# Kernel tuning notes

Hardware: AMD Instinct MI355X
Metric: run time of the kernel (lower is better)

The kernel has to match this reference:

```python
import jax, jax.numpy as jnp
import numpy as np
import math

MIN_NORM = 1e-15
EPS = 4e-3  # float32 boundary eps used by PoincareBall.proj
C = 1.0


def artanh(x):
    x = jnp.clip(x, -1.0 + 1e-7, 1.0 - 1e-7)
    return 0.5 * (jnp.log1p(x) - jnp.log1p(-x))


def _norm(x):
    return jnp.maximum(jnp.linalg.norm(x, axis=-1, keepdims=True), MIN_NORM)


def proj(x, c):
    n = _norm(x)
    maxnorm = (1.0 - EPS) / jnp.sqrt(c)
    return jnp.where(n > maxnorm, x / n * maxnorm, x)


def expmap0(u, c):
    sc = jnp.sqrt(c)
    n = _norm(u)
    return jnp.tanh(sc * n) * u / (sc * n)


def logmap0(p, c):
    sc = jnp.sqrt(c)
    n = _norm(p)
    return artanh(sc * n) * p / (sc * n)


def mobius_add(x, y, c):
    x2 = jnp.sum(x * x, -1, keepdims=True)
    y2 = jnp.sum(y * y, -1, keepdims=True)
    xy = jnp.sum(x * y, -1, keepdims=True)
    num = (1 + 2 * c * xy + c * y2) * x + (1 - c * x2) * y
    den = 1 + 2 * c * xy + c * c * x2 * y2
    return num / jnp.maximum(den, MIN_NORM)


def mobius_matvec(m, x, c):
    sc = jnp.sqrt(c)
    xn = _norm(x)
    mx = x @ m.T
    mxn = _norm(mx)
    res = jnp.tanh(mxn / xn * artanh(sc * xn)) * mx / (mxn * sc)
    zero = jnp.all(mx == 0, axis=-1, keepdims=True)
    return jnp.where(zero, jnp.zeros((), x.dtype), res)


def hnn_layer(x, W, b, c):
    # HypLinear (dropout=0, use_bias=1) followed by HypAct(relu); proj_tan0 is identity for PoincareBall.
    res = proj(mobius_matvec(W, x, c), c)
    hb = proj(expmap0(b.reshape(1, -1), c), c)
    res = proj(mobius_add(res, hb, c), c)
    xt = jax.nn.relu(logmap0(res, c))
    return proj(expmap0(xt, c), c)


def setup_inputs():
    key = jax.random.key(0)
    ks = jax.random.split(key, 5)
    B, N, K, D = 4, 2000, 5, 32
    H1, H2 = 160, 32  # H_layer1: 32 -> 32*5, H_layer2: 32 -> 32
    # points on the Poincare ball (small norm so logmap0 is well-conditioned)
    in_feats = 0.05 * jax.random.normal(ks[0], (B, N, D), jnp.float32)
    # one-hot neighbor adjacency [batch, agent, nei, agent]
    nei_idx = jax.random.randint(ks[1], (B, N, K), 0, N)
    in_nei = jax.nn.one_hot(nei_idx, N, dtype=jnp.float32)
    # xavier_uniform with gain sqrt(2), zero bias (reset_parameters)
    b1w = math.sqrt(2.0) * math.sqrt(6.0 / (H1 + D))
    b2w = math.sqrt(2.0) * math.sqrt(6.0 / (H2 + H2))
    W1 = jax.random.uniform(ks[2], (H1, D), jnp.float32, -b1w, b1w)
    W2 = jax.random.uniform(ks[3], (H2, H2), jnp.float32, -b2w, b2w)
    b1 = jnp.zeros((H1,), jnp.float32)
    b2 = jnp.zeros((H2,), jnp.float32)
    return {"in_feats": in_feats, "in_nei": in_nei, "W1": W1, "b1": b1,
            "W2": W2, "b2": b2, "h_dim": 32, "head": 5}


def reference(in_feats, in_nei, W1, b1, W2, b2, h_dim, head):
    c = C
    B, N, D = in_feats.shape
    K = in_nei.shape[2]
    # tangent-space features (proj_tan0 is identity)
    feats = logmap0(in_feats, c)                                   # [B,N,D]
    agent = proj(expmap0(feats[:, :, None, :], c), c)              # [B,N,1,D]
    # one-hot adjacency gather: equals matmul(in_nei, repeat(feats)) in the torch code
    nbr_t = jnp.einsum('bnkm,bmd->bnkd', in_nei, feats)            # [B,N,K,D]
    nbr = proj(expmap0(nbr_t, c), c)
    # query heads
    q = logmap0(hnn_layer(agent, W1, b1, c), c)                    # [B,N,1,h*head]
    q = q.reshape(B, N, 1, h_dim, head).transpose(0, 1, 4, 2, 3)   # [B,N,head,1,h]
    # key heads; the torch code recomputes H_layer1(neighbor_repr) for values with
    # identical weights/inputs (dropout=0), so values == keys and we reuse them.
    kv = logmap0(hnn_layer(nbr, W1, b1, c), c)
    kv = kv.reshape(B, N, K, h_dim, head).transpose(0, 1, 4, 2, 3)  # [B,N,head,K,h]
    att = jax.nn.softmax(jnp.einsum('bnhqd,bnhkd->bnhqk', q, kv), axis=-1)  # [B,N,head,1,K]
    att_record = att.reshape(B, N, head, K)
    out = jnp.einsum('bnhqk,bnhkd->bnhqd', att, kv).mean(axis=2)   # [B,N,1,h]
    out = out.reshape(B, N, h_dim)
    out = proj(expmap0(out, c), c)
    out = hnn_layer(out, W2, b2, c)                                # [B,N,32]
    return out, att_record
```

## Files before the change

### kernel.cpp

```cpp
#include <hip/hip_runtime.h>
#include <math.h>

#define BB 4
#define NN 2000
#define KK 5
#define DD 32
#define H1 160
#define HEAD 5
#define HDIM 32
#define MAXNORM 0.996f
#define MINN 1e-15f

__device__ __forceinline__ float artanh_f(float x) {
    x = fminf(fmaxf(x, -1.0f + 1e-7f), 1.0f - 1e-7f);
    return 0.5f * (log1pf(x) - log1pf(-x));
}

__device__ __forceinline__ float wave_sum(float v) {
#pragma unroll
    for (int o = 32; o > 0; o >>= 1) v += __shfl_xor(v, o, 64);
    return v;
}

__global__ __launch_bounds__(256) void find_idx_kernel(const float* __restrict__ nei,
                                                       int* __restrict__ idx) {
    const int total4 = BB * NN * KK * NN / 4;
    int stride = gridDim.x * blockDim.x;
    for (int i = blockIdx.x * blockDim.x + threadIdx.x; i < total4; i += stride) {
        float4 v = ((const float4*)nei)[i];
        int f = -1;
        if (v.x > 0.5f) f = 0;
        if (v.y > 0.5f) f = 1;
        if (v.z > 0.5f) f = 2;
        if (v.w > 0.5f) f = 3;
        if (f >= 0) {
            int flat = i * 4 + f;
            int row = flat / NN;
            int m = flat - row * NN;
            idx[row] = m;
        }
    }
}

__global__ __launch_bounds__(256) void g_kernel(const float* __restrict__ xin,
                                                const float* __restrict__ W1,
                                                const float* __restrict__ b1,
                                                float* __restrict__ g) {
    int wave = (blockIdx.x * blockDim.x + threadIdx.x) >> 6;
    int lane = threadIdx.x & 63;
    if (wave >= BB * NN) return;
    bool j2ok = lane < (H1 - 128);

    float x = (lane < DD) ? xin[wave * DD + lane] : 0.f;

    float n = fmaxf(sqrtf(wave_sum(x * x)), MINN);
    float f = (artanh_f(n) / n) * x;
    float fn = fmaxf(sqrtf(wave_sum(f * f)), MINN);
    float p = (tanhf(fn) / fn) * f;
    float pn = fmaxf(sqrtf(wave_sum(p * p)), MINN);
    if (pn > MAXNORM) p *= MAXNORM / pn;
    float xn = fmaxf(sqrtf(wave_sum(p * p)), MINN);

    float mx0 = 0.f, mx1 = 0.f, mx2 = 0.f;
#pragma unroll
    for (int d = 0; d < DD; ++d) {
        float pd = __shfl(p, d, 64);
        mx0 += W1[lane * DD + d] * pd;
        mx1 += W1[(lane + 64) * DD + d] * pd;
        if (j2ok) mx2 += W1[(lane + 128) * DD + d] * pd;
    }
    float m2 = mx0 * mx0 + mx1 * mx1 + (j2ok ? mx2 * mx2 : 0.f);
    float mxn = fmaxf(sqrtf(wave_sum(m2)), MINN);
    float sc = tanhf(mxn / xn * artanh_f(xn)) / mxn;
    float r0 = sc * mx0, r1 = sc * mx1, r2 = sc * mx2;
    float rn = fmaxf(sqrtf(wave_sum(r0 * r0 + r1 * r1 + (j2ok ? r2 * r2 : 0.f))), MINN);
    if (rn > MAXNORM) { float s = MAXNORM / rn; r0 *= s; r1 *= s; r2 *= s; }

    float bb0 = b1[lane], bb1 = b1[lane + 64], bb2 = j2ok ? b1[lane + 128] : 0.f;
    float bn = fmaxf(sqrtf(wave_sum(bb0 * bb0 + bb1 * bb1 + bb2 * bb2)), MINN);
    float bs = tanhf(bn) / bn;
    float h0 = bs * bb0, h1 = bs * bb1, h2 = bs * bb2;
    float hn = fmaxf(sqrtf(wave_sum(h0 * h0 + h1 * h1 + h2 * h2)), MINN);
    if (hn > MAXNORM) { float s = MAXNORM / hn; h0 *= s; h1 *= s; h2 *= s; }

    float x2s = wave_sum(r0 * r0 + r1 * r1 + (j2ok ? r2 * r2 : 0.f));
    float y2s = wave_sum(h0 * h0 + h1 * h1 + h2 * h2);
    float xys = wave_sum(r0 * h0 + r1 * h1 + (j2ok ? r2 * h2 : 0.f));
    float ca = 1.f + 2.f * xys + y2s;
    float cb = 1.f - x2s;
    float den = fmaxf(1.f + 2.f * xys + x2s * y2s, MINN);
    float a0 = (ca * r0 + cb * h0) / den;
    float a1 = (ca * r1 + cb * h1) / den;
    float a2 = (ca * r2 + cb * h2) / den;
    float an = fmaxf(sqrtf(wave_sum(a0 * a0 + a1 * a1 + (j2ok ? a2 * a2 : 0.f))), MINN);
    if (an > MAXNORM) { float s = MAXNORM / an; a0 *= s; a1 *= s; a2 *= s; }

    float ln = fmaxf(sqrtf(wave_sum(a0 * a0 + a1 * a1 + (j2ok ? a2 * a2 : 0.f))), MINN);
    float ls = artanh_f(ln) / ln;
    float t0 = fmaxf(ls * a0, 0.f), t1 = fmaxf(ls * a1, 0.f), t2 = fmaxf(ls * a2, 0.f);
    float tn = fmaxf(sqrtf(wave_sum(t0 * t0 + t1 * t1 + (j2ok ? t2 * t2 : 0.f))), MINN);
    float es = tanhf(tn) / tn;
    float y0 = es * t0, y1 = es * t1, y2 = es * t2;
    float yn = fmaxf(sqrtf(wave_sum(y0 * y0 + y1 * y1 + (j2ok ? y2 * y2 : 0.f))), MINN);
    if (yn > MAXNORM) { float s = MAXNORM / yn; y0 *= s; y1 *= s; y2 *= s; }
    float gn = fmaxf(sqrtf(wave_sum(y0 * y0 + y1 * y1 + (j2ok ? y2 * y2 : 0.f))), MINN);
    float gs = artanh_f(gn) / gn;

    float* go = g + (size_t)wave * H1;
    go[lane] = gs * y0;
    go[lane + 64] = gs * y1;
    if (j2ok) go[lane + 128] = gs * y2;
}

__global__ __launch_bounds__(256) void att_kernel(const float* __restrict__ g,
                                                  const int* __restrict__ idx,
                                                  float* __restrict__ att_out) {
    int t = blockIdx.x * blockDim.x + threadIdx.x;
    if (t >= BB * NN * HEAD) return;
    int h = t % HEAD;
    int r = t / HEAD;
    int b = r / NN;

    const float* gq = g + (size_t)r * H1;
    float q[HDIM];
#pragma unroll
    for (int d = 0; d < HDIM; ++d) q[d] = gq[d * HEAD + h];

    float s[KK];
#pragma unroll
    for (int k = 0; k < KK; ++k) {
        int m = idx[r * KK + k];
        const float* gk = g + (size_t)(b * NN + m) * H1;
        float acc = 0.f;
#pragma unroll
        for (int d = 0; d < HDIM; ++d) acc += q[d] * gk[d * HEAD + h];
        s[k] = acc;
    }
    float mxv = s[0];
#pragma unroll
    for (int k = 1; k < KK; ++k) mxv = fmaxf(mxv, s[k]);
    float e[KK], sum = 0.f;
#pragma unroll
    for (int k = 0; k < KK; ++k) { e[k] = expf(s[k] - mxv); sum += e[k]; }
    float inv = 1.f / sum;
#pragma unroll
    for (int k = 0; k < KK; ++k) att_out[t * KK + k] = e[k] * inv;
}

__global__ __launch_bounds__(256) void out_kernel(const float* __restrict__ g,
                                                  const int* __restrict__ idx,
                                                  const float* __restrict__ att,
                                                  const float* __restrict__ W2,
                                                  const float* __restrict__ b2,
                                                  float* __restrict__ out) {
    int r = blockIdx.x * blockDim.x + threadIdx.x;
    if (r >= BB * NN) return;
    int b = r / NN;

    float o[HDIM];
#pragma unroll
    for (int d = 0; d < HDIM; ++d) o[d] = 0.f;
#pragma unroll
    for (int k = 0; k < KK; ++k) {
        int m = idx[r * KK + k];
        const float* gk = g + (size_t)(b * NN + m) * H1;
#pragma unroll
        for (int h = 0; h < HEAD; ++h) {
            float a = att[(r * HEAD + h) * KK + k];
#pragma unroll
            for (int d = 0; d < HDIM; ++d) o[d] += a * gk[d * HEAD + h];
        }
    }
#pragma unroll
    for (int d = 0; d < HDIM; ++d) o[d] *= (1.f / HEAD);

    float n2 = 0.f;
#pragma unroll
    for (int d = 0; d < HDIM; ++d) n2 += o[d] * o[d];
    float n = fmaxf(sqrtf(n2), MINN);
    float es = tanhf(n) / n;
#pragma unroll
    for (int d = 0; d < HDIM; ++d) o[d] *= es;
    n2 = 0.f;
#pragma unroll
    for (int d = 0; d < HDIM; ++d) n2 += o[d] * o[d];
    n = fmaxf(sqrtf(n2), MINN);
    if (n > MAXNORM) {
        float s = MAXNORM / n;
#pragma unroll
        for (int d = 0; d < HDIM; ++d) o[d] *= s;
    }

    float xn2 = 0.f;
#pragma unroll
    for (int d = 0; d < HDIM; ++d) xn2 += o[d] * o[d];
    float xn = fmaxf(sqrtf(xn2), MINN);
    float mx[HDIM];
#pragma unroll
    for (int j = 0; j < HDIM; ++j) {
        float acc = 0.f;
#pragma unroll
        for (int d = 0; d < HDIM; ++d) acc += W2[j * HDIM + d] * o[d];
        mx[j] = acc;
    }
    float mxn2 = 0.f;
#pragma unroll
    for (int j = 0; j < HDIM; ++j) mxn2 += mx[j] * mx[j];
    float mxn = fmaxf(sqrtf(mxn2), MINN);
    float sc = tanhf(mxn / xn * artanh_f(xn)) / mxn;
#pragma unroll
    for (int j = 0; j < HDIM; ++j) mx[j] *= sc;
    float rn2 = 0.f;
#pragma unroll
    for (int j = 0; j < HDIM; ++j) rn2 += mx[j] * mx[j];
    float rn = fmaxf(sqrtf(rn2), MINN);
    if (rn > MAXNORM) {
        float s = MAXNORM / rn;
#pragma unroll
        for (int j = 0; j < HDIM; ++j) mx[j] *= s;
    }

    float hb[HDIM];
    float bn2 = 0.f;
#pragma unroll
    for (int j = 0; j < HDIM; ++j) { hb[j] = b2[j]; bn2 += hb[j] * hb[j]; }
    float bn = fmaxf(sqrtf(bn2), MINN);
    float bs = tanhf(bn) / bn;
    float hn2 = 0.f;
#pragma unroll
    for (int j = 0; j < HDIM; ++j) { hb[j] *= bs; hn2 += hb[j] * hb[j]; }
    float hn = fmaxf(sqrtf(hn2), MINN);
    if (hn > MAXNORM) {
        float s = MAXNORM / hn;
#pragma unroll
        for (int j = 0; j < HDIM; ++j) hb[j] *= s;
    }
    float x2s = 0.f, y2s = 0.f, xys = 0.f;
#pragma unroll
    for (int j = 0; j < HDIM; ++j) {
        x2s += mx[j] * mx[j];
        y2s += hb[j] * hb[j];
        xys += mx[j] * hb[j];
    }
    float ca = 1.f + 2.f * xys + y2s;
    float cb = 1.f - x2s;
    float den = fmaxf(1.f + 2.f * xys + x2s * y2s, MINN);
    float a[HDIM];
#pragma unroll
    for (int j = 0; j < HDIM; ++j) a[j] = (ca * mx[j] + cb * hb[j]) / den;
    float an2 = 0.f;
#pragma unroll
    for (int j = 0; j < HDIM; ++j) an2 += a[j] * a[j];
    float an = fmaxf(sqrtf(an2), MINN);
    if (an > MAXNORM) {
        float s = MAXNORM / an;
#pragma unroll
        for (int j = 0; j < HDIM; ++j) a[j] *= s;
    }
    float ln2 = 0.f;
#pragma unroll
    for (int j = 0; j < HDIM; ++j) ln2 += a[j] * a[j];
    float lnn = fmaxf(sqrtf(ln2), MINN);
    float ls = artanh_f(lnn) / lnn;
#pragma unroll
    for (int j = 0; j < HDIM; ++j) a[j] = fmaxf(ls * a[j], 0.f);
    float tn2 = 0.f;
#pragma unroll
    for (int j = 0; j < HDIM; ++j) tn2 += a[j] * a[j];
    float tn = fmaxf(sqrtf(tn2), MINN);
    float es2 = tanhf(tn) / tn;
#pragma unroll
    for (int j = 0; j < HDIM; ++j) a[j] *= es2;
    float yn2 = 0.f;
#pragma unroll
    for (int j = 0; j < HDIM; ++j) yn2 += a[j] * a[j];
    float yn = fmaxf(sqrtf(yn2), MINN);
    if (yn > MAXNORM) {
        float s = MAXNORM / yn;
#pragma unroll
        for (int j = 0; j < HDIM; ++j) a[j] *= s;
    }
#pragma unroll
    for (int j = 0; j < HDIM; ++j) out[(size_t)r * HDIM + j] = a[j];
}

extern "C" void kernel_launch(void* const* d_in, const int* in_sizes, int n_in,
                              void* d_out, int out_size, void* d_ws, size_t ws_size,
                              hipStream_t stream) {
    const float* in_feats = (const float*)d_in[0];
    const float* in_nei = (const float*)d_in[1];
    const float* W1 = (const float*)d_in[2];
    const float* b1 = (const float*)d_in[3];
    const float* W2 = (const float*)d_in[4];
    const float* b2 = (const float*)d_in[5];

    int* idx = (int*)d_ws;
    size_t idx_bytes = ((size_t)BB * NN * KK * sizeof(int) + 255) & ~(size_t)255;
    float* g = (float*)((char*)d_ws + idx_bytes);

    float* out = (float*)d_out;
    float* att = out + (size_t)BB * NN * HDIM;

    hipLaunchKernelGGL(find_idx_kernel, dim3(4096), dim3(256), 0, stream, in_nei, idx);
    hipLaunchKernelGGL(g_kernel, dim3((BB * NN * 64 + 255) / 256), dim3(256), 0, stream,
                       in_feats, W1, b1, g);
    hipLaunchKernelGGL(att_kernel, dim3((BB * NN * HEAD + 255) / 256), dim3(256), 0, stream,
                       g, idx, att);
    hipLaunchKernelGGL(out_kernel, dim3((BB * NN + 255) / 256), dim3(256), 0, stream,
                       g, idx, att, W2, b2, out);
}
```

Baseline: 594.8 us.

## Fuse attention and output kernels wave-per-row; early-exit one-hot index search

Merges the attention-softmax kernel and the output kernel into one kernel that uses a 64-lane wave per agent row. The 32 feature dimensions are spread across lanes and reduced with cross-lane shuffles, replacing per-thread 32-element register arrays and strided gathers. The intermediate attention buffer is no longer written and re-read. The index finder now assigns one wave per one-hot row and stops at the first chunk holding the 1, which avoids scanning the rest of the adjacency row. That early exit assumes each row contains exactly one nonzero.

```diff
diff --git a/kernel.cpp b/kernel.cpp
--- a/kernel.cpp
+++ b/kernel.cpp
@@ -22,22 +22,34 @@
     return v;
 }
 
+__device__ __forceinline__ float wave_sum32(float v) {
+#pragma unroll
+    for (int o = 16; o > 0; o >>= 1) v += __shfl_xor(v, o, 64);
+    return v;
+}
+
 __global__ __launch_bounds__(256) void find_idx_kernel(const float* __restrict__ nei,
                                                        int* __restrict__ idx) {
-    const int total4 = BB * NN * KK * NN / 4;
-    int stride = gridDim.x * blockDim.x;
-    for (int i = blockIdx.x * blockDim.x + threadIdx.x; i < total4; i += stride) {
-        float4 v = ((const float4*)nei)[i];
-        int f = -1;
-        if (v.x > 0.5f) f = 0;
-        if (v.y > 0.5f) f = 1;
-        if (v.z > 0.5f) f = 2;
-        if (v.w > 0.5f) f = 3;
-        if (f >= 0) {
-            int flat = i * 4 + f;
-            int row = flat / NN;
-            int m = flat - row * NN;
-            idx[row] = m;
+    int wave = (blockIdx.x * blockDim.x + threadIdx.x) >> 6;
+    int lane = threadIdx.x & 63;
+    if (wave >= BB * NN * KK) return;
+    const float* row = nei + (size_t)wave * NN;
+#pragma unroll 1
+    for (int it = 0; it < 8; ++it) {
+        int base = it * 256 + lane * 4;
+        bool found = false;
+        int pos = 0;
+        if (base < NN) {
+            float4 v = *(const float4*)(row + base);
+            if (v.x > 0.5f) { found = true; pos = base; }
+            if (v.y > 0.5f) { found = true; pos = base + 1; }
+            if (v.z > 0.5f) { found = true; pos = base + 2; }
+            if (v.w > 0.5f) { found = true; pos = base + 3; }
+        }
+        unsigned long long m = __ballot(found);
+        if (m) {
+            if (found) idx[wave] = pos;
+            break;
         }
     }
 }
@@ -112,176 +124,103 @@
     if (j2ok) go[lane + 128] = gs * y2;
 }
 
-__global__ __launch_bounds__(256) void att_kernel(const float* __restrict__ g,
-                                                  const int* __restrict__ idx,
-                                                  float* __restrict__ att_out) {
-    int t = blockIdx.x * blockDim.x + threadIdx.x;
-    if (t >= BB * NN * HEAD) return;
-    int h = t % HEAD;
-    int r = t / HEAD;
+__global__ __launch_bounds__(256) void fused_att_out_kernel(const float* __restrict__ g,
+                                                            const int* __restrict__ idx,
+                                                            const float* __restrict__ W2,
+                                                            const float* __restrict__ b2,
+                                                            float* __restrict__ out,
+                                                            float* __restrict__ att_out) {
+    int wave = (blockIdx.x * blockDim.x + threadIdx.x) >> 6;
+    int lane = threadIdx.x & 63;
+    if (wave >= BB * NN) return;
+    int r = wave;
     int b = r / NN;
+    int d = lane & 31;
 
     const float* gq = g + (size_t)r * H1;
-    float q[HDIM];
-#pragma unroll
-    for (int d = 0; d < HDIM; ++d) q[d] = gq[d * HEAD + h];
-
-    float s[KK];
+    float q[HEAD];
+#pragma unroll
+    for (int h = 0; h < HEAD; ++h) q[h] = gq[d * HEAD + h];
+
+    float kv[KK][HEAD];
+    float s[KK][HEAD];
 #pragma unroll
     for (int k = 0; k < KK; ++k) {
         int m = idx[r * KK + k];
         const float* gk = g + (size_t)(b * NN + m) * H1;
-        float acc = 0.f;
-#pragma unroll
-        for (int d = 0; d < HDIM; ++d) acc += q[d] * gk[d * HEAD + h];
-        s[k] = acc;
-    }
-    float mxv = s[0];
-#pragma unroll
-    for (int k = 1; k < KK; ++k) mxv = fmaxf(mxv, s[k]);
-    float e[KK], sum = 0.f;
-#pragma unroll
-    for (int k = 0; k < KK; ++k) { e[k] = expf(s[k] - mxv); sum += e[k]; }
-    float inv = 1.f / sum;
-#pragma unroll
-    for (int k = 0; k < KK; ++k) att_out[t * KK + k] = e[k] * inv;
-}
-
-__global__ __launch_bounds__(256) void out_kernel(const float* __restrict__ g,
-                                                  const int* __restrict__ idx,
-                                                  const float* __restrict__ att,
-                                                  const float* __restrict__ W2,
-                                                  const float* __restrict__ b2,
-                                                  float* __restrict__ out) {
-    int r = blockIdx.x * blockDim.x + threadIdx.x;
-    if (r >= BB * NN) return;
-    int b = r / NN;
-
-    float o[HDIM];
-#pragma unroll
-    for (int d = 0; d < HDIM; ++d) o[d] = 0.f;
-#pragma unroll
-    for (int k = 0; k < KK; ++k) {
-        int m = idx[r * KK + k];
-        const float* gk = g + (size_t)(b * NN + m) * H1;
-#pragma unroll
-        for (int h = 0; h < HEAD; ++h) {
-            float a = att[(r * HEAD + h) * KK + k];
-#pragma unroll
-            for (int d = 0; d < HDIM; ++d) o[d] += a * gk[d * HEAD + h];
-        }
-    }
-#pragma unroll
-    for (int d = 0; d < HDIM; ++d) o[d] *= (1.f / HEAD);
-
-    float n2 = 0.f;
-#pragma unroll
-    for (int d = 0; d < HDIM; ++d) n2 += o[d] * o[d];
-    float n = fmaxf(sqrtf(n2), MINN);
-    float es = tanhf(n) / n;
-#pragma unroll
-    for (int d = 0; d < HDIM; ++d) o[d] *= es;
-    n2 = 0.f;
-#pragma unroll
-    for (int d = 0; d < HDIM; ++d) n2 += o[d] * o[d];
-    n = fmaxf(sqrtf(n2), MINN);
-    if (n > MAXNORM) {
-        float s = MAXNORM / n;
-#pragma unroll
-        for (int d = 0; d < HDIM; ++d) o[d] *= s;
-    }
-
-    float xn2 = 0.f;
-#pragma unroll
-    for (int d = 0; d < HDIM; ++d) xn2 += o[d] * o[d];
-    float xn = fmaxf(sqrtf(xn2), MINN);
-    float mx[HDIM];
-#pragma unroll
-    for (int j = 0; j < HDIM; ++j) {
-        float acc = 0.f;
-#pragma unroll
-        for (int d = 0; d < HDIM; ++d) acc += W2[j * HDIM + d] * o[d];
-        mx[j] = acc;
-    }
-    float mxn2 = 0.f;
-#pragma unroll
-    for (int j = 0; j < HDIM; ++j) mxn2 += mx[j] * mx[j];
-    float mxn = fmaxf(sqrtf(mxn2), MINN);
+#pragma unroll
+        for (int h = 0; h < HEAD; ++h) kv[k][h] = gk[d * HEAD + h];
+#pragma unroll
+        for (int h = 0; h < HEAD; ++h) s[k][h] = wave_sum32(q[h] * kv[k][h]);
+    }
+
+    float att[HEAD][KK];
+#pragma unroll
+    for (int h = 0; h < HEAD; ++h) {
+        float mxv = s[0][h];
+#pragma unroll
+        for (int k = 1; k < KK; ++k) mxv = fmaxf(mxv, s[k][h]);
+        float sum = 0.f;
+#pragma unroll
+        for (int k = 0; k < KK; ++k) { att[h][k] = expf(s[k][h] - mxv); sum += att[h][k]; }
+        float inv = 1.f / sum;
+#pragma unroll
+        for (int k = 0; k < KK; ++k) att[h][k] *= inv;
+    }
+    if (lane < HEAD * KK) {
+        int h = lane / KK, k = lane % KK;
+        att_out[(size_t)r * HEAD * KK + lane] = att[h][k];
+    }
+
+    float o = 0.f;
+#pragma unroll
+    for (int h = 0; h < HEAD; ++h)
+#pragma unroll
+        for (int k = 0; k < KK; ++k) o += att[h][k] * kv[k][h];
+    o *= (1.f / HEAD);
+
+    float n = fmaxf(sqrtf(wave_sum32(o * o)), MINN);
+    o *= tanhf(n) / n;
+    n = fmaxf(sqrtf(wave_sum32(o * o)), MINN);
+    if (n > MAXNORM) o *= MAXNORM / n;
+
+    float xn = fmaxf(sqrtf(wave_sum32(o * o)), MINN);
+    float mx = 0.f;
+#pragma unroll
+    for (int dd = 0; dd < HDIM; ++dd) {
+        float od = __shfl(o, dd, 64);
+        mx += W2[d * HDIM + dd] * od;
+    }
+    float mxn = fmaxf(sqrtf(wave_sum32(mx * mx)), MINN);
     float sc = tanhf(mxn / xn * artanh_f(xn)) / mxn;
-#pragma unroll
-    for (int j = 0; j < HDIM; ++j) mx[j] *= sc;
-    float rn2 = 0.f;
-#pragma unroll
-    for (int j = 0; j < HDIM; ++j) rn2 += mx[j] * mx[j];
-    float rn = fmaxf(sqrtf(rn2), MINN);
-    if (rn > MAXNORM) {
-        float s = MAXNORM / rn;
-#pragma unroll
-        for (int j = 0; j < HDIM; ++j) mx[j] *= s;
-    }
-
-    float hb[HDIM];
-    float bn2 = 0.f;
-#pragma unroll
-    for (int j = 0; j < HDIM; ++j) { hb[j] = b2[j]; bn2 += hb[j] * hb[j]; }
-    float bn = fmaxf(sqrtf(bn2), MINN);
-    float bs = tanhf(bn) / bn;
-    float hn2 = 0.f;
-#pragma unroll
-    for (int j = 0; j < HDIM; ++j) { hb[j] *= bs; hn2 += hb[j] * hb[j]; }
-    float hn = fmaxf(sqrtf(hn2), MINN);
-    if (hn > MAXNORM) {
-        float s = MAXNORM / hn;
-#pragma unroll
-        for (int j = 0; j < HDIM; ++j) hb[j] *= s;
-    }
-    float x2s = 0.f, y2s = 0.f, xys = 0.f;
-#pragma unroll
-    for (int j = 0; j < HDIM; ++j) {
-        x2s += mx[j] * mx[j];
-        y2s += hb[j] * hb[j];
-        xys += mx[j] * hb[j];
-    }
+    mx *= sc;
+    float rn = fmaxf(sqrtf(wave_sum32(mx * mx)), MINN);
+    if (rn > MAXNORM) mx *= MAXNORM / rn;
+
+    float hb = b2[d];
+    float bn = fmaxf(sqrtf(wave_sum32(hb * hb)), MINN);
+    hb *= tanhf(bn) / bn;
+    float hn = fmaxf(sqrtf(wave_sum32(hb * hb)), MINN);
+    if (hn > MAXNORM) hb *= MAXNORM / hn;
+
+    float x2s = wave_sum32(mx * mx);
+    float y2s = wave_sum32(hb * hb);
+    float xys = wave_sum32(mx * hb);
     float ca = 1.f + 2.f * xys + y2s;
     float cb = 1.f - x2s;
     float den = fmaxf(1.f + 2.f * xys + x2s * y2s, MINN);
-    float a[HDIM];
-#pragma unroll
-    for (int j = 0; j < HDIM; ++j) a[j] = (ca * mx[j] + cb * hb[j]) / den;
-    float an2 = 0.f;
-#pragma unroll
-    for (int j = 0; j < HDIM; ++j) an2 += a[j] * a[j];
-    float an = fmaxf(sqrtf(an2), MINN);
-    if (an > MAXNORM) {
-        float s = MAXNORM / an;
-#pragma unroll
-        for (int j = 0; j < HDIM; ++j) a[j] *= s;
-    }
-    float ln2 = 0.f;
-#pragma unroll
-    for (int j = 0; j < HDIM; ++j) ln2 += a[j] * a[j];
-    float lnn = fmaxf(sqrtf(ln2), MINN);
-    float ls = artanh_f(lnn) / lnn;
-#pragma unroll
-    for (int j = 0; j < HDIM; ++j) a[j] = fmaxf(ls * a[j], 0.f);
-    float tn2 = 0.f;
-#pragma unroll
-    for (int j = 0; j < HDIM; ++j) tn2 += a[j] * a[j];
-    float tn = fmaxf(sqrtf(tn2), MINN);
-    float es2 = tanhf(tn) / tn;
-#pragma unroll
-    for (int j = 0; j < HDIM; ++j) a[j] *= es2;
-    float yn2 = 0.f;
-#pragma unroll
-    for (int j = 0; j < HDIM; ++j) yn2 += a[j] * a[j];
-    float yn = fmaxf(sqrtf(yn2), MINN);
-    if (yn > MAXNORM) {
-        float s = MAXNORM / yn;
-#pragma unroll
-        for (int j = 0; j < HDIM; ++j) a[j] *= s;
-    }
-#pragma unroll
-    for (int j = 0; j < HDIM; ++j) out[(size_t)r * HDIM + j] = a[j];
+    float a = (ca * mx + cb * hb) / den;
+    float an = fmaxf(sqrtf(wave_sum32(a * a)), MINN);
+    if (an > MAXNORM) a *= MAXNORM / an;
+
+    float ln = fmaxf(sqrtf(wave_sum32(a * a)), MINN);
+    a = fmaxf((artanh_f(ln) / ln) * a, 0.f);
+    float tn = fmaxf(sqrtf(wave_sum32(a * a)), MINN);
+    a *= tanhf(tn) / tn;
+    float yn = fmaxf(sqrtf(wave_sum32(a * a)), MINN);
+    if (yn > MAXNORM) a *= MAXNORM / yn;
+
+    if (lane < HDIM) out[(size_t)r * HDIM + lane] = a;
 }
 
 extern "C" void kernel_launch(void* const* d_in, const int* in_sizes, int n_in,
@@ -301,11 +240,10 @@
     float* out = (float*)d_out;
     float* att = out + (size_t)BB * NN * HDIM;
 
-    hipLaunchKernelGGL(find_idx_kernel, dim3(4096), dim3(256), 0, stream, in_nei, idx);
+    hipLaunchKernelGGL(find_idx_kernel, dim3(BB * NN * KK * 64 / 256), dim3(256), 0, stream,
+                       in_nei, idx);
     hipLaunchKernelGGL(g_kernel, dim3((BB * NN * 64 + 255) / 256), dim3(256), 0, stream,
                        in_feats, W1, b1, g);
-    hipLaunchKernelGGL(att_kernel, dim3((BB * NN * HEAD + 255) / 256), dim3(256), 0, stream,
-                       g, idx, att);
-    hipLaunchKernelGGL(out_kernel, dim3((BB * NN + 255) / 256), dim3(256), 0, stream,
-                       g, idx, att, W2, b2, out);
-}
+    hipLaunchKernelGGL(fused_att_out_kernel, dim3((BB * NN * 64 + 255) / 256), dim3(256), 0, stream,
+                       g, idx, W2, b2, out, att);
+}
```

Measured after the change: 520.8 us. -12.4%, faster.
